# Kernel optimization log

Measured on AMD Instinct MI355X. Metric: run time of the kernel, lower is better.

The kernel has to match this reference:

```python
import jax, jax.numpy as jnp
import numpy as np

N_ATOMS = 500000
MUL0, MUL1, MUL2 = 32, 16, 8      # geometry/output multiplicities for 0e,1o,2e
FMUL0, FMUL1 = 32, 16             # field multiplicities for 0e,1o

# real Wigner 3j for (1,1,2) in e3nn real basis order (l=1: y,z,x ; l=2: xy,yz,z2,zx,x2-y2)
# orthonormal symmetric-traceless basis matrices / sqrt(5) so that sum of squares == 1
def _w3j_112():
    s2 = 1.0 / np.sqrt(2.0); s6 = 1.0 / np.sqrt(6.0)
    C = np.zeros((3, 3, 5), np.float32)
    C[0, 2, 0] = C[2, 0, 0] = s2            # xy
    C[0, 1, 1] = C[1, 0, 1] = s2            # yz
    C[1, 1, 2] = 2.0 * s6; C[0, 0, 2] = -s6; C[2, 2, 2] = -s6  # z2
    C[1, 2, 3] = C[2, 1, 3] = s2            # zx
    C[2, 2, 4] = s2; C[0, 0, 4] = -s2       # x2-y2
    return C / np.sqrt(5.0)

W3J112 = jnp.asarray(_w3j_112())
INV_S3 = float(1.0 / np.sqrt(3.0))   # w3j(0,l,l) = I/sqrt(2l+1), w3j(1,1,0) = I/sqrt(3)
INV_S5 = float(1.0 / np.sqrt(5.0))   # w3j(2,0,2) = I/sqrt(5)
# e3nn FullyConnectedTensorProduct path coefficients (component irrep_normalization, element path_normalization):
# sqrt((2*l_out+1) / sum over paths with same output of mul1*mul2)
C0 = float(np.sqrt(1.0 / (MUL0 * FMUL0 + MUL1 * FMUL1)))          # -> 0e : 1/sqrt(1280)
C1 = float(np.sqrt(3.0 / (MUL0 * FMUL1 + MUL1 * FMUL0 + MUL2 * FMUL1)))  # -> 1o : sqrt(3/1152)
C2 = float(np.sqrt(5.0 / (MUL1 * FMUL1 + MUL2 * FMUL0)))          # -> 2e : sqrt(5/512)


def _forward(geometry_features, field_features,
             w_000, w_011, w_101, w_110, w_112, w_202, w_211,
             wl0, wl1, wl2):
    n = geometry_features.shape[0]
    g0 = geometry_features[:, :32]                       # (n, 32)
    g1 = geometry_features[:, 32:80].reshape(n, 16, 3)   # (n, 16, 3)
    g2 = geometry_features[:, 80:120].reshape(n, 8, 5)   # (n, 8, 5)
    f0 = field_features[:32]                             # (32,)  global, broadcast over atoms
    f1 = field_features[32:].reshape(16, 3)              # (16, 3)

    # --- tensor product paths (uvw connection mode) ---
    out0 = C0 * (jnp.einsum('uvw,zu,v->zw', w_000, g0, f0)
                 + INV_S3 * jnp.einsum('uvw,zui,vi->zw', w_110, g1, f1))
    out1 = C1 * (INV_S3 * jnp.einsum('uvw,zu,vk->zwk', w_011, g0, f1)
                 + INV_S3 * jnp.einsum('uvw,zuk,v->zwk', w_101, g1, f0)
                 + jnp.einsum('uvw,ijk,zuk,vi->zwj', w_211, W3J112, g2, f1))
    out2 = C2 * (jnp.einsum('uvw,ijk,zui,vj->zwk', w_112, W3J112, g1, f1)
                 + INV_S5 * jnp.einsum('uvw,zuk,v->zwk', w_202, g2, f0))

    # --- residual o3.Linear (matching irreps only, 1/sqrt(fan_in)) ---
    r0 = jnp.einsum('uw,zu->zw', wl0, g0) * float(1.0 / np.sqrt(MUL0))
    r1 = jnp.einsum('uw,zui->zwi', wl1, g1) * float(1.0 / np.sqrt(MUL1))
    r2 = jnp.einsum('uw,zui->zwi', wl2, g2) * float(1.0 / np.sqrt(MUL2))

    return jnp.concatenate([out0 + r0,
                            (out1 + r1).reshape(n, 48),
                            (out2 + r2).reshape(n, 40)], axis=1)


def setup_inputs() -> dict:
    key = jax.random.key(0)
    ks = jax.random.split(key, 12)
    rn = lambda k, s: jax.random.normal(k, s, dtype=jnp.float32)
    return {
        'geometry_features': rn(ks[0], (N_ATOMS, 120)),
        'field_features': rn(ks[1], (80,)),
        'w_000': rn(ks[2], (32, 32, 32)),  # (0e,0e)->0e
        'w_011': rn(ks[3], (32, 16, 16)),  # (0e,1o)->1o
        'w_101': rn(ks[4], (16, 32, 16)),  # (1o,0e)->1o
        'w_110': rn(ks[5], (16, 16, 32)),  # (1o,1o)->0e
        'w_112': rn(ks[6], (16, 16, 8)),   # (1o,1o)->2e
        'w_202': rn(ks[7], (8, 32, 8)),    # (2e,0e)->2e
        'w_211': rn(ks[8], (8, 16, 16)),   # (2e,1o)->1o
        'wl0': rn(ks[9], (32, 32)),
        'wl1': rn(ks[10], (16, 16)),
        'wl2': rn(ks[11], (8, 8)),
    }


def reference(geometry_features, field_features,
              w_000, w_011, w_101, w_110, w_112, w_202, w_211,
              wl0, wl1, wl2):
    return _forward(geometry_features, field_features,
                    w_000, w_011, w_101, w_110, w_112, w_202, w_211,
                    wl0, wl1, wl2)
```

## Files before the change

kernel.cpp:

```cpp
#include <hip/hip_runtime.h>

#define LDA 136
#define TM  64

__constant__ float W3J[45] = {
  0.f, 0.f, -0.18257418583505536f, 0.f, -0.31622776601683794f,
  0.f, 0.31622776601683794f, 0.f, 0.f, 0.f,
  0.31622776601683794f, 0.f, 0.f, 0.f, 0.f,
  0.f, 0.31622776601683794f, 0.f, 0.f, 0.f,
  0.f, 0.f, 0.36514837167011072f, 0.f, 0.f,
  0.f, 0.f, 0.f, 0.31622776601683794f, 0.f,
  0.31622776601683794f, 0.f, 0.f, 0.f, 0.f,
  0.f, 0.f, 0.f, 0.31622776601683794f, 0.f,
  0.f, 0.f, -0.18257418583505536f, 0.f, 0.31622776601683794f
};

__device__ __forceinline__ unsigned short f2bf(float f) {
  unsigned int u = __float_as_uint(f);
  u += 0x7FFFu + ((u >> 16) & 1u);
  return (unsigned short)(u >> 16);
}

__global__ void build_B_kernel(
    const float* __restrict__ field,
    const float* __restrict__ w000, const float* __restrict__ w011,
    const float* __restrict__ w101, const float* __restrict__ w110,
    const float* __restrict__ w112, const float* __restrict__ w202,
    const float* __restrict__ w211, const float* __restrict__ wl0,
    const float* __restrict__ wl1,  const float* __restrict__ wl2,
    unsigned short* __restrict__ Bt)
{
  const float C0  = 0.02795084971874737f;
  const float C1  = 0.051031036307982884f;
  const float C2  = 0.09882117688026186f;
  const float IS3 = 0.57735026918962576f;
  const float IS5 = 0.44721359549995794f;

  int n = blockIdx.x;
  int k = threadIdx.x;
  float val = 0.0f;

  if (n < 120 && k < 120) {
    if (n < 32) {
      int w = n;
      if (k < 32) {
        int u = k;
        float a = 0.f;
        for (int v = 0; v < 32; ++v) a += w000[u*1024 + v*32 + w] * field[v];
        val = C0 * a + wl0[u*32 + w] * 0.17677669529663689f;
      } else if (k < 80) {
        int u = (k-32)/3, i = (k-32)%3;
        float a = 0.f;
        for (int v = 0; v < 16; ++v) a += w110[u*512 + v*32 + w] * field[32 + v*3 + i];
        val = C0 * IS3 * a;
      }
    } else if (n < 80) {
      int w = (n-32)/3, j = (n-32)%3;
      if (k < 32) {
        int u = k;
        float a = 0.f;
        for (int v = 0; v < 16; ++v) a += w011[u*256 + v*16 + w] * field[32 + v*3 + j];
        val = C1 * IS3 * a;
      } else if (k < 80) {
        int u = (k-32)/3, i = (k-32)%3;
        if (i == j) {
          float a = 0.f;
          for (int v = 0; v < 32; ++v) a += w101[u*512 + v*16 + w] * field[v];
          val = C1 * IS3 * a + wl1[u*16 + w] * 0.25f;
        }
      } else {
        int u = (k-80)/5, kk = (k-80)%5;
        float c0w = W3J[0*15 + j*5 + kk];
        float c1w = W3J[1*15 + j*5 + kk];
        float c2w = W3J[2*15 + j*5 + kk];
        float a = 0.f;
        for (int v = 0; v < 16; ++v) {
          float s = c0w*field[32+v*3+0] + c1w*field[32+v*3+1] + c2w*field[32+v*3+2];
          a += w211[u*256 + v*16 + w] * s;
        }
        val = C1 * a;
      }
    } else {
      int w = (n-80)/5, k2 = (n-80)%5;
      if (k >= 32 && k < 80) {
        int u = (k-32)/3, i = (k-32)%3;
        float c0w = W3J[i*15 + 0*5 + k2];
        float c1w = W3J[i*15 + 1*5 + k2];
        float c2w = W3J[i*15 + 2*5 + k2];
        float a = 0.f;
        for (int v = 0; v < 16; ++v) {
          float s = c0w*field[32+v*3+0] + c1w*field[32+v*3+1] + c2w*field[32+v*3+2];
          a += w112[u*128 + v*8 + w] * s;
        }
        val = C2 * a;
      } else if (k >= 80) {
        int u = (k-80)/5, kk = (k-80)%5;
        if (kk == k2) {
          float a = 0.f;
          for (int v = 0; v < 32; ++v) a += w202[u*256 + v*8 + w] * field[v];
          val = C2 * IS5 * a + wl2[u*8 + w] * 0.35355339059327378f;
        }
      }
    }
  }
  Bt[n*128 + k] = f2bf(val);
}

typedef __attribute__((ext_vector_type(8))) __bf16 bf16x8;
typedef __attribute__((ext_vector_type(4))) float  f32x4;

__global__ __launch_bounds__(256) void coupling_main(
    const float* __restrict__ geom, const unsigned short* __restrict__ Btg,
    float* __restrict__ out, int natoms)
{
  __shared__ alignas(16) unsigned short Alds[TM  * LDA];
  __shared__ alignas(16) unsigned short Blds[128 * LDA];

  int tid = threadIdx.x;
  long long base = (long long)blockIdx.x * TM;

  #pragma unroll
  for (int r = 0; r < 8; ++r) {
    int g   = tid + r * 256;
    int row = g >> 4;
    int col = (g & 15) * 8;
    uint4 v = ((const uint4*)Btg)[g];
    *((uint4*)&Blds[row * LDA + col]) = v;
  }
  if (tid < TM) {
    *((uint4*)&Alds[tid * LDA + 120]) = make_uint4(0u, 0u, 0u, 0u);
  }
  #pragma unroll
  for (int r = 0; r < 4; ++r) {
    int g = tid + r * 256;
    if (g < 960) {
      int row = g / 15;
      int col = (g - row * 15) * 8;
      long long atom = base + row;
      uint4 pk;
      if (atom < natoms) {
        const float* src = geom + (long long)atom * 120 + col;
        float4 fa = ((const float4*)src)[0];
        float4 fb = ((const float4*)src)[1];
        pk.x = ((unsigned)f2bf(fa.y) << 16) | f2bf(fa.x);
        pk.y = ((unsigned)f2bf(fa.w) << 16) | f2bf(fa.z);
        pk.z = ((unsigned)f2bf(fb.y) << 16) | f2bf(fb.x);
        pk.w = ((unsigned)f2bf(fb.w) << 16) | f2bf(fb.z);
      } else {
        pk = make_uint4(0u, 0u, 0u, 0u);
      }
      *((uint4*)&Alds[row * LDA + col]) = pk;
    }
  }
  __syncthreads();

  int lane = tid & 63;
  int wave = tid >> 6;
  int mrow = lane & 15;
  int kq   = lane >> 4;

  f32x4 zero = {0.f, 0.f, 0.f, 0.f};
  f32x4 acc[8];
  #pragma unroll
  for (int t = 0; t < 8; ++t) acc[t] = zero;

  const unsigned short* arow = &Alds[(wave * 16 + mrow) * LDA + kq * 8];
  const unsigned short* brow = &Blds[mrow * LDA + kq * 8];

  #pragma unroll
  for (int ks = 0; ks < 4; ++ks) {
    bf16x8 af = __builtin_bit_cast(bf16x8, *(const uint4*)(arow + ks * 32));
    #pragma unroll
    for (int t = 0; t < 8; ++t) {
      bf16x8 bf_ = __builtin_bit_cast(bf16x8, *(const uint4*)(brow + t * 16 * LDA + ks * 32));
      acc[t] = __builtin_amdgcn_mfma_f32_16x16x32_bf16(af, bf_, acc[t], 0, 0, 0);
    }
  }

  long long atom0 = base + wave * 16 + kq * 4;
  #pragma unroll
  for (int t = 0; t < 8; ++t) {
    int n = t * 16 + mrow;
    if (n < 120) {
      #pragma unroll
      for (int r2 = 0; r2 < 4; ++r2) {
        long long atom = atom0 + r2;
        if (atom < natoms) out[atom * 120 + n] = acc[t][r2];
      }
    }
  }
}

extern "C" void kernel_launch(void* const* d_in, const int* in_sizes, int n_in,
                              void* d_out, int out_size, void* d_ws, size_t ws_size,
                              hipStream_t stream) {
  const float* geom  = (const float*)d_in[0];
  const float* field = (const float*)d_in[1];
  const float* w000  = (const float*)d_in[2];
  const float* w011  = (const float*)d_in[3];
  const float* w101  = (const float*)d_in[4];
  const float* w110  = (const float*)d_in[5];
  const float* w112  = (const float*)d_in[6];
  const float* w202  = (const float*)d_in[7];
  const float* w211  = (const float*)d_in[8];
  const float* wl0   = (const float*)d_in[9];
  const float* wl1   = (const float*)d_in[10];
  const float* wl2   = (const float*)d_in[11];
  float* out = (float*)d_out;
  unsigned short* Bt = (unsigned short*)d_ws;

  int natoms = in_sizes[0] / 120;

  build_B_kernel<<<dim3(128), dim3(128), 0, stream>>>(
      field, w000, w011, w101, w110, w112, w202, w211, wl0, wl1, wl2, Bt);

  int ntiles = (natoms + TM - 1) / TM;
  coupling_main<<<dim3(ntiles), dim3(256), 0, stream>>>(geom, Bt, out, natoms);
}
```

Baseline: 420.4 us.

## Pre-swizzle B into MFMA fragment layout and load A directly into registers

The weight matrix is now written by the build kernel in the exact per-lane MFMA fragment order, so the main kernel copies it linearly into LDS and reads one 16-byte vector per fragment with no padding. The geometry tile no longer goes through LDS: each lane loads its own A fragment straight from global memory and converts it to bf16 in registers. The change also adds nontemporal loads and stores and a launch-bounds occupancy hint. This removes the LDS staging of A and halves the LDS footprint, at the cost of less coalesced per-lane global loads for A.

```diff
diff --git a/kernel.cpp b/kernel.cpp
--- a/kernel.cpp
+++ b/kernel.cpp
@@ -1,7 +1,4 @@
 #include <hip/hip_runtime.h>
-
-#define LDA 136
-#define TM  64
 
 __constant__ float W3J[45] = {
   0.f, 0.f, -0.18257418583505536f, 0.f, -0.31622776601683794f,
@@ -28,7 +25,7 @@
     const float* __restrict__ w112, const float* __restrict__ w202,
     const float* __restrict__ w211, const float* __restrict__ wl0,
     const float* __restrict__ wl1,  const float* __restrict__ wl2,
-    unsigned short* __restrict__ Bt)
+    unsigned short* __restrict__ Bf)
 {
   const float C0  = 0.02795084971874737f;
   const float C1  = 0.051031036307982884f;
@@ -36,8 +33,8 @@
   const float IS3 = 0.57735026918962576f;
   const float IS5 = 0.44721359549995794f;
 
-  int n = blockIdx.x;
-  int k = threadIdx.x;
+  int k = blockIdx.x;
+  int n = threadIdx.x;
   float val = 0.0f;
 
   if (n < 120 && k < 120) {
@@ -103,76 +100,64 @@
       }
     }
   }
-  Bt[n*128 + k] = f2bf(val);
+  int t  = n >> 4;
+  int ks = k >> 5;
+  int lane = ((k >> 3) & 3) * 16 + (n & 15);
+  int j  = k & 7;
+  Bf[(((t*4 + ks)*64 + lane) << 3) + j] = f2bf(val);
 }
 
 typedef __attribute__((ext_vector_type(8))) __bf16 bf16x8;
 typedef __attribute__((ext_vector_type(4))) float  f32x4;
-
-__global__ __launch_bounds__(256) void coupling_main(
-    const float* __restrict__ geom, const unsigned short* __restrict__ Btg,
+typedef __attribute__((ext_vector_type(4))) unsigned int u32x4;
+
+__global__ __launch_bounds__(256, 4) void coupling_main(
+    const float* __restrict__ geom, const u32x4* __restrict__ Bfg,
     float* __restrict__ out, int natoms)
 {
-  __shared__ alignas(16) unsigned short Alds[TM  * LDA];
-  __shared__ alignas(16) unsigned short Blds[128 * LDA];
+  __shared__ u32x4 Blds[2048];
 
   int tid = threadIdx.x;
-  long long base = (long long)blockIdx.x * TM;
-
   #pragma unroll
   for (int r = 0; r < 8; ++r) {
-    int g   = tid + r * 256;
-    int row = g >> 4;
-    int col = (g & 15) * 8;
-    uint4 v = ((const uint4*)Btg)[g];
-    *((uint4*)&Blds[row * LDA + col]) = v;
-  }
-  if (tid < TM) {
-    *((uint4*)&Alds[tid * LDA + 120]) = make_uint4(0u, 0u, 0u, 0u);
-  }
-  #pragma unroll
-  for (int r = 0; r < 4; ++r) {
     int g = tid + r * 256;
-    if (g < 960) {
-      int row = g / 15;
-      int col = (g - row * 15) * 8;
-      long long atom = base + row;
-      uint4 pk;
-      if (atom < natoms) {
-        const float* src = geom + (long long)atom * 120 + col;
-        float4 fa = ((const float4*)src)[0];
-        float4 fb = ((const float4*)src)[1];
-        pk.x = ((unsigned)f2bf(fa.y) << 16) | f2bf(fa.x);
-        pk.y = ((unsigned)f2bf(fa.w) << 16) | f2bf(fa.z);
-        pk.z = ((unsigned)f2bf(fb.y) << 16) | f2bf(fb.x);
-        pk.w = ((unsigned)f2bf(fb.w) << 16) | f2bf(fb.z);
-      } else {
-        pk = make_uint4(0u, 0u, 0u, 0u);
-      }
-      *((uint4*)&Alds[row * LDA + col]) = pk;
-    }
+    Blds[g] = Bfg[g];
   }
   __syncthreads();
 
   int lane = tid & 63;
   int wave = tid >> 6;
-  int mrow = lane & 15;
+  int nl   = lane & 15;
   int kq   = lane >> 4;
+
+  long long base  = (long long)blockIdx.x * 64;
+  long long atomA = base + wave * 16 + nl;
+  bool av = atomA < natoms;
+  const f32x4* ap = (const f32x4*)(geom + atomA * 120);
 
   f32x4 zero = {0.f, 0.f, 0.f, 0.f};
   f32x4 acc[8];
   #pragma unroll
   for (int t = 0; t < 8; ++t) acc[t] = zero;
 
-  const unsigned short* arow = &Alds[(wave * 16 + mrow) * LDA + kq * 8];
-  const unsigned short* brow = &Blds[mrow * LDA + kq * 8];
-
   #pragma unroll
   for (int ks = 0; ks < 4; ++ks) {
-    bf16x8 af = __builtin_bit_cast(bf16x8, *(const uint4*)(arow + ks * 32));
+    f32x4 fa = zero;
+    f32x4 fb = zero;
+    if (av && !(ks == 3 && kq == 3)) {
+      fa = __builtin_nontemporal_load(&ap[ks * 8 + kq * 2]);
+      fb = __builtin_nontemporal_load(&ap[ks * 8 + kq * 2 + 1]);
+    }
+    u32x4 pk;
+    pk.x = ((unsigned)f2bf(fa.y) << 16) | f2bf(fa.x);
+    pk.y = ((unsigned)f2bf(fa.w) << 16) | f2bf(fa.z);
+    pk.z = ((unsigned)f2bf(fb.y) << 16) | f2bf(fb.x);
+    pk.w = ((unsigned)f2bf(fb.w) << 16) | f2bf(fb.z);
+    bf16x8 af = __builtin_bit_cast(bf16x8, pk);
+
     #pragma unroll
     for (int t = 0; t < 8; ++t) {
-      bf16x8 bf_ = __builtin_bit_cast(bf16x8, *(const uint4*)(brow + t * 16 * LDA + ks * 32));
+      bf16x8 bf_ = __builtin_bit_cast(bf16x8, Blds[(t * 4 + ks) * 64 + lane]);
       acc[t] = __builtin_amdgcn_mfma_f32_16x16x32_bf16(af, bf_, acc[t], 0, 0, 0);
     }
   }
@@ -180,12 +165,13 @@
   long long atom0 = base + wave * 16 + kq * 4;
   #pragma unroll
   for (int t = 0; t < 8; ++t) {
-    int n = t * 16 + mrow;
+    int n = t * 16 + nl;
     if (n < 120) {
       #pragma unroll
       for (int r2 = 0; r2 < 4; ++r2) {
         long long atom = atom0 + r2;
-        if (atom < natoms) out[atom * 120 + n] = acc[t][r2];
+        if (atom < natoms)
+          __builtin_nontemporal_store(acc[t][r2], &out[atom * 120 + n]);
       }
     }
   }
@@ -207,13 +193,14 @@
   const float* wl1   = (const float*)d_in[10];
   const float* wl2   = (const float*)d_in[11];
   float* out = (float*)d_out;
-  unsigned short* Bt = (unsigned short*)d_ws;
+  unsigned short* Bf = (unsigned short*)d_ws;
 
   int natoms = in_sizes[0] / 120;
 
   build_B_kernel<<<dim3(128), dim3(128), 0, stream>>>(
-      field, w000, w011, w101, w110, w112, w202, w211, wl0, wl1, wl2, Bt);
-
-  int ntiles = (natoms + TM - 1) / TM;
-  coupling_main<<<dim3(ntiles), dim3(256), 0, stream>>>(geom, Bt, out, natoms);
-}
+      field, w000, w011, w101, w110, w112, w202, w211, wl0, wl1, wl2, Bf);
+
+  int ntiles = (natoms + 63) / 64;
+  coupling_main<<<dim3(ntiles), dim3(256), 0, stream>>>(
+      geom, (const u32x4*)Bf, out, natoms);
+}
```

Measured after the change: 514.1 us. +22.3%, slower.
